# Optimization experiments

Measured on AMD Instinct MI355X. Metric: run time of the kernel, lower is better.

The kernel has to match this reference:

```python
import jax, jax.numpy as jnp
import numpy as np

N_QUBITS = 13
N_LAYERS = 8
DIM = 2 ** N_QUBITS
CDT = jnp.complex64

_X = jnp.array([[0.0, 1.0], [1.0, 0.0]], dtype=CDT)
_Z = jnp.array([[1.0, 0.0], [0.0, -1.0]], dtype=CDT)
_I2 = jnp.eye(2, dtype=CDT)
_CNOT = jnp.array([[1, 0, 0, 0], [0, 1, 0, 0], [0, 0, 0, 1], [0, 0, 1, 0]], dtype=CDT)


def build_ops():
    """Hardware-efficient ansatz: per layer RX on all qubits, RZ on all qubits, CNOT chain."""
    ops = []
    p = 0
    for _ in range(N_LAYERS):
        for q in range(N_QUBITS):
            ops.append(('RX', (q,), p)); p += 1
        for q in range(N_QUBITS):
            ops.append(('RZ', (q,), p)); p += 1
        for q in range(N_QUBITS - 1):
            ops.append(('CNOT', (q, q + 1), None))
    return ops, p

OPS, N_PARAMS = build_ops()


def _rot(generator, theta):
    # U = cos(theta/2) I - i sin(theta/2) G
    h = theta * 0.5
    return jnp.cos(h).astype(CDT) * _I2 - 1j * jnp.sin(h).astype(CDT) * generator


def _apply_1q(state, U, q):
    st = state.reshape((2,) * N_QUBITS)
    st = jnp.tensordot(U, st, axes=([1], [q]))  # contracted axis moves to front
    return jnp.moveaxis(st, 0, q).reshape(-1)


def _apply_2q(state, U, q0, q1):
    st = state.reshape((2,) * N_QUBITS)
    st = jnp.tensordot(U.reshape(2, 2, 2, 2), st, axes=([2, 3], [q0, q1]))
    return jnp.moveaxis(st, (0, 1), (q0, q1)).reshape(-1)


def _run_circuit(params):
    state = jnp.zeros(DIM, dtype=CDT).at[0].set(1.0)
    for gate, qubits, pidx in OPS:
        if gate == 'RX':
            state = _apply_1q(state, _rot(_X, params[pidx]), qubits[0])
        elif gate == 'RZ':
            state = _apply_1q(state, _rot(_Z, params[pidx]), qubits[0])
        else:  # CNOT
            state = _apply_2q(state, _CNOT, qubits[0], qubits[1])
    return state


def setup_inputs() -> dict:
    key = jax.random.key(0)
    k1, k2 = jax.random.split(key)
    params = jax.random.normal(k1, (N_PARAMS,), dtype=jnp.float32)
    observable = jax.random.normal(k2, (DIM, DIM), dtype=jnp.float32)
    return {"params": params, "observable": observable}


def reference(params, observable) -> jnp.ndarray:
    psi = _run_circuit(params)                      # [2^n] complex64
    obs_psi = observable.astype(CDT) @ psi          # dense observable matvec
    loss = jnp.vdot(psi, obs_psi).real.astype(jnp.float32)  # <psi|O|psi>
    return loss
```

## Files before the change

kernel.cpp:

```cpp
#include <hip/hip_runtime.h>

#define DIM 8192
#define NLAYERS 8
#define SIMT 512
#define QFB 2048
#define QFT 256
#define ROWS_PER_BLOCK 4

typedef float floatx4 __attribute__((ext_vector_type(4)));

__device__ __forceinline__ int swz(int i) { return i ^ ((i >> 4) & 15); }

__global__ __launch_bounds__(SIMT) void sim_kernel(const float* __restrict__ params,
                                                   float* __restrict__ outR,
                                                   float* __restrict__ outM) {
    __shared__ float2 buf[2][DIM];
    const int t = threadIdx.x;

    float2 a[16];
#pragma unroll
    for (int l = 0; l < 16; ++l) a[l] = make_float2(0.f, 0.f);
    if (t == 0) a[0].x = 1.f;

    int pp = 0;

    for (int layer = 0; layer < NLAYERS; ++layer) {
        const float* __restrict__ prx = params + layer * 26;
        const float* __restrict__ prz = prx + 13;

        float cb[13], sb[13];
#pragma unroll
        for (int p = 0; p < 13; ++p) __sincosf(0.5f * prx[12 - p], &sb[p], &cb[p]);

#pragma unroll
        for (int k = 0; k < 4; ++k) {
            const float c = cb[k], s = sb[k];
#pragma unroll
            for (int l0 = 0; l0 < 16; ++l0) {
                if (!(l0 & (1 << k))) {
                    const int l1 = l0 | (1 << k);
                    const float2 a0 = a[l0], a1 = a[l1];
                    a[l0] = make_float2(fmaf(c, a0.x, s * a1.y), fmaf(c, a0.y, -s * a1.x));
                    a[l1] = make_float2(fmaf(c, a1.x, s * a0.y), fmaf(c, a1.y, -s * a0.x));
                }
            }
        }

        {
            float2* __restrict__ B = buf[pp]; pp ^= 1;
#pragma unroll
            for (int l = 0; l < 16; ++l) B[swz((t << 4) | l)] = a[l];
            __syncthreads();
#pragma unroll
            for (int l = 0; l < 16; ++l) a[l] = B[swz((t & 15) | (l << 4) | ((t >> 4) << 8))];
        }

#pragma unroll
        for (int k = 0; k < 4; ++k) {
            const float c = cb[4 + k], s = sb[4 + k];
#pragma unroll
            for (int l0 = 0; l0 < 16; ++l0) {
                if (!(l0 & (1 << k))) {
                    const int l1 = l0 | (1 << k);
                    const float2 a0 = a[l0], a1 = a[l1];
                    a[l0] = make_float2(fmaf(c, a0.x, s * a1.y), fmaf(c, a0.y, -s * a1.x));
                    a[l1] = make_float2(fmaf(c, a1.x, s * a0.y), fmaf(c, a1.y, -s * a0.x));
                }
            }
        }

        {
            float2* __restrict__ B = buf[pp]; pp ^= 1;
#pragma unroll
            for (int l = 0; l < 16; ++l) B[swz((t & 15) | (l << 4) | ((t >> 4) << 8))] = a[l];
            __syncthreads();
#pragma unroll
            for (int l = 0; l < 16; ++l)
                a[l] = B[swz(((t >> 1) & 255) | (l << 8) | ((t & 1) << 12))];
        }

#pragma unroll
        for (int k = 0; k < 4; ++k) {
            const float c = cb[8 + k], s = sb[8 + k];
#pragma unroll
            for (int l0 = 0; l0 < 16; ++l0) {
                if (!(l0 & (1 << k))) {
                    const int l1 = l0 | (1 << k);
                    const float2 a0 = a[l0], a1 = a[l1];
                    a[l0] = make_float2(fmaf(c, a0.x, s * a1.y), fmaf(c, a0.y, -s * a1.x));
                    a[l1] = make_float2(fmaf(c, a1.x, s * a0.y), fmaf(c, a1.y, -s * a0.x));
                }
            }
        }

        {
            const float c = cb[12], s = sb[12];
#pragma unroll
            for (int l = 0; l < 16; ++l) {
                const float ox = __shfl_xor(a[l].x, 1);
                const float oy = __shfl_xor(a[l].y, 1);
                a[l] = make_float2(fmaf(c, a[l].x, s * oy), fmaf(c, a[l].y, -s * ox));
            }
        }

        float hz[13];
#pragma unroll
        for (int p = 0; p < 13; ++p) hz[p] = 0.5f * prz[12 - p];
        float phiT = 0.f;
#pragma unroll
        for (int p = 0; p < 8; ++p) phiT += (((t >> 1) >> p) & 1) ? hz[p] : -hz[p];
        phiT += (t & 1) ? hz[12] : -hz[12];
#pragma unroll
        for (int l = 0; l < 16; ++l) {
            float phi = phiT;
            phi += (l & 1) ? hz[8]  : -hz[8];
            phi += (l & 2) ? hz[9]  : -hz[9];
            phi += (l & 4) ? hz[10] : -hz[10];
            phi += (l & 8) ? hz[11] : -hz[11];
            float sp, cp;
            __sincosf(phi, &sp, &cp);
            a[l] = make_float2(a[l].x * cp - a[l].y * sp, a[l].x * sp + a[l].y * cp);
        }

        {
            float2* __restrict__ B = buf[pp]; pp ^= 1;
#pragma unroll
            for (int l = 0; l < 16; ++l)
                B[swz(((t >> 1) & 255) | (l << 8) | ((t & 1) << 12))] = a[l];
            __syncthreads();
#pragma unroll
            for (int l = 0; l < 16; ++l) {
                const int c0 = (t << 4) | l;
                a[l] = B[swz(c0 ^ (c0 >> 1))];
            }
        }
    }

#pragma unroll
    for (int g = 0; g < 4; ++g) {
        const float4 rv = make_float4(a[4*g].x, a[4*g+1].x, a[4*g+2].x, a[4*g+3].x);
        const float4 mv = make_float4(a[4*g].y, a[4*g+1].y, a[4*g+2].y, a[4*g+3].y);
        ((float4*)outR)[(t << 2) + g] = rv;
        ((float4*)outM)[(t << 2) + g] = mv;
    }
}

__global__ __launch_bounds__(QFT) void quad_kernel(const float* __restrict__ O,
                                                   const float* __restrict__ R,
                                                   const float* __restrict__ M,
                                                   float* __restrict__ partials) {
    const int bi = blockIdx.x;
    const int t  = threadIdx.x;
    const float4* __restrict__ R4 = (const float4*)R;
    const float4* __restrict__ M4 = (const float4*)M;

    float acc = 0.f;
#pragma unroll
    for (int rr = 0; rr < ROWS_PER_BLOCK; ++rr) {
        const int i = bi * ROWS_PER_BLOCK + rr;
        const float ri = R[i];
        const float mi = M[i];
        const floatx4* __restrict__ Or = (const floatx4*)(O + (size_t)i * DIM);
#pragma unroll
        for (int it = 0; it < DIM / 4 / QFT; ++it) {
            const int j4 = t + it * QFT;
            const floatx4 o = __builtin_nontemporal_load(&Or[j4]);
            const float4 rj = R4[j4];
            const float4 mj = M4[j4];
            acc = fmaf(o.x, fmaf(ri, rj.x, mi * mj.x), acc);
            acc = fmaf(o.y, fmaf(ri, rj.y, mi * mj.y), acc);
            acc = fmaf(o.z, fmaf(ri, rj.z, mi * mj.z), acc);
            acc = fmaf(o.w, fmaf(ri, rj.w, mi * mj.w), acc);
        }
    }

#pragma unroll
    for (int off = 32; off > 0; off >>= 1) acc += __shfl_down(acc, off);
    __shared__ float wsum[QFT / 64];
    const int lane = t & 63, w = t >> 6;
    if (lane == 0) wsum[w] = acc;
    __syncthreads();
    if (t == 0) {
        float s = 0.f;
#pragma unroll
        for (int k = 0; k < QFT / 64; ++k) s += wsum[k];
        partials[bi] = s;
    }
}

__global__ __launch_bounds__(256) void reduce_kernel(const float* __restrict__ partials,
                                                     float* __restrict__ out) {
    const int t = threadIdx.x;
    float acc = 0.f;
#pragma unroll
    for (int k = 0; k < QFB / 256; ++k) acc += partials[t + k * 256];
#pragma unroll
    for (int off = 32; off > 0; off >>= 1) acc += __shfl_down(acc, off);
    __shared__ float wsum[4];
    const int lane = t & 63, w = t >> 6;
    if (lane == 0) wsum[w] = acc;
    __syncthreads();
    if (t == 0) out[0] = wsum[0] + wsum[1] + wsum[2] + wsum[3];
}

extern "C" void kernel_launch(void* const* d_in, const int* in_sizes, int n_in,
                              void* d_out, int out_size, void* d_ws, size_t ws_size,
                              hipStream_t stream) {
    const float* params = (const float*)d_in[0];
    const float* O      = (const float*)d_in[1];
    float* out = (float*)d_out;

    float* R        = (float*)d_ws;
    float* M        = R + DIM;
    float* partials = M + DIM;

    sim_kernel<<<1, SIMT, 0, stream>>>(params, R, M);
    quad_kernel<<<QFB, QFT, 0, stream>>>(O, R, M, partials);
    reduce_kernel<<<1, 256, 0, stream>>>(partials, out);
}
```

Measured before the change: 83.99 us.

## Fuse simulation and quadratic form into one cooperative kernel with L2 prefetch

Merges the three kernels into a single cooperative launch. Block 0 runs the state-vector simulation while the other blocks stream the tail of the observable matrix (rows from 2048 on) to warm the cache. After a grid sync, every block computes the quadratic form over 32 rows using register-cached psi and separate real and imaginary dot products, and a second grid sync leads to the final reduction. This hides the serial simulation latency behind observable loading and removes launch gaps, but it relies on the prefetched data surviving in cache and on cooperative grid synchronisation.

```diff
diff --git a/kernel.cpp b/kernel.cpp
--- a/kernel.cpp
+++ b/kernel.cpp
@@ -1,206 +1,220 @@
 #include <hip/hip_runtime.h>
+#include <hip/hip_cooperative_groups.h>
 
 #define DIM 8192
 #define NLAYERS 8
-#define SIMT 512
-#define QFB 2048
-#define QFT 256
-#define ROWS_PER_BLOCK 4
-
-typedef float floatx4 __attribute__((ext_vector_type(4)));
+#define NB 256
+#define NT 512
+#define ROWS_PB (DIM / NB)
+#define PRIME_ROW0 2048
+
+namespace cg = cooperative_groups;
 
 __device__ __forceinline__ int swz(int i) { return i ^ ((i >> 4) & 15); }
 
-__global__ __launch_bounds__(SIMT) void sim_kernel(const float* __restrict__ params,
-                                                   float* __restrict__ outR,
-                                                   float* __restrict__ outM) {
-    __shared__ float2 buf[2][DIM];
-    const int t = threadIdx.x;
-
-    float2 a[16];
-#pragma unroll
-    for (int l = 0; l < 16; ++l) a[l] = make_float2(0.f, 0.f);
-    if (t == 0) a[0].x = 1.f;
-
-    int pp = 0;
-
-    for (int layer = 0; layer < NLAYERS; ++layer) {
-        const float* __restrict__ prx = params + layer * 26;
-        const float* __restrict__ prz = prx + 13;
-
-        float cb[13], sb[13];
-#pragma unroll
-        for (int p = 0; p < 13; ++p) __sincosf(0.5f * prx[12 - p], &sb[p], &cb[p]);
-
-#pragma unroll
-        for (int k = 0; k < 4; ++k) {
-            const float c = cb[k], s = sb[k];
-#pragma unroll
-            for (int l0 = 0; l0 < 16; ++l0) {
-                if (!(l0 & (1 << k))) {
-                    const int l1 = l0 | (1 << k);
-                    const float2 a0 = a[l0], a1 = a[l1];
-                    a[l0] = make_float2(fmaf(c, a0.x, s * a1.y), fmaf(c, a0.y, -s * a1.x));
-                    a[l1] = make_float2(fmaf(c, a1.x, s * a0.y), fmaf(c, a1.y, -s * a0.x));
-                }
-            }
-        }
-
-        {
-            float2* __restrict__ B = buf[pp]; pp ^= 1;
-#pragma unroll
-            for (int l = 0; l < 16; ++l) B[swz((t << 4) | l)] = a[l];
-            __syncthreads();
-#pragma unroll
-            for (int l = 0; l < 16; ++l) a[l] = B[swz((t & 15) | (l << 4) | ((t >> 4) << 8))];
-        }
-
-#pragma unroll
-        for (int k = 0; k < 4; ++k) {
-            const float c = cb[4 + k], s = sb[4 + k];
-#pragma unroll
-            for (int l0 = 0; l0 < 16; ++l0) {
-                if (!(l0 & (1 << k))) {
-                    const int l1 = l0 | (1 << k);
-                    const float2 a0 = a[l0], a1 = a[l1];
-                    a[l0] = make_float2(fmaf(c, a0.x, s * a1.y), fmaf(c, a0.y, -s * a1.x));
-                    a[l1] = make_float2(fmaf(c, a1.x, s * a0.y), fmaf(c, a1.y, -s * a0.x));
-                }
-            }
-        }
-
-        {
-            float2* __restrict__ B = buf[pp]; pp ^= 1;
-#pragma unroll
-            for (int l = 0; l < 16; ++l) B[swz((t & 15) | (l << 4) | ((t >> 4) << 8))] = a[l];
+__global__ __launch_bounds__(NT, 2) void fused_kernel(const float* __restrict__ params,
+                                                      const float* __restrict__ O,
+                                                      float* __restrict__ R,
+                                                      float* __restrict__ M,
+                                                      float* __restrict__ partials,
+                                                      float* __restrict__ out) {
+    __shared__ float2 buf[DIM];
+    __shared__ float wsum[8];
+    const int t   = threadIdx.x;
+    const int bid = blockIdx.x;
+    cg::grid_group grid = cg::this_grid();
+
+    if (bid == 0) {
+        float2 a[16];
+#pragma unroll
+        for (int l = 0; l < 16; ++l) a[l] = make_float2(0.f, 0.f);
+        if (t == 0) a[0].x = 1.f;
+
+        for (int layer = 0; layer < NLAYERS; ++layer) {
+            const float* __restrict__ prx = params + layer * 26;
+            const float* __restrict__ prz = prx + 13;
+
+            float cb[13], sb[13];
+#pragma unroll
+            for (int p = 0; p < 13; ++p) __sincosf(0.5f * prx[12 - p], &sb[p], &cb[p]);
+
+#pragma unroll
+            for (int k = 0; k < 4; ++k) {
+                const float c = cb[k], s = sb[k];
+#pragma unroll
+                for (int l0 = 0; l0 < 16; ++l0) {
+                    if (!(l0 & (1 << k))) {
+                        const int l1 = l0 | (1 << k);
+                        const float2 a0 = a[l0], a1 = a[l1];
+                        a[l0] = make_float2(fmaf(c, a0.x, s * a1.y), fmaf(c, a0.y, -s * a1.x));
+                        a[l1] = make_float2(fmaf(c, a1.x, s * a0.y), fmaf(c, a1.y, -s * a0.x));
+                    }
+                }
+            }
+
+            __syncthreads();
+#pragma unroll
+            for (int l = 0; l < 16; ++l) buf[swz((t << 4) | l)] = a[l];
+            __syncthreads();
+#pragma unroll
+            for (int l = 0; l < 16; ++l) a[l] = buf[swz((t & 15) | (l << 4) | ((t >> 4) << 8))];
+
+#pragma unroll
+            for (int k = 0; k < 4; ++k) {
+                const float c = cb[4 + k], s = sb[4 + k];
+#pragma unroll
+                for (int l0 = 0; l0 < 16; ++l0) {
+                    if (!(l0 & (1 << k))) {
+                        const int l1 = l0 | (1 << k);
+                        const float2 a0 = a[l0], a1 = a[l1];
+                        a[l0] = make_float2(fmaf(c, a0.x, s * a1.y), fmaf(c, a0.y, -s * a1.x));
+                        a[l1] = make_float2(fmaf(c, a1.x, s * a0.y), fmaf(c, a1.y, -s * a0.x));
+                    }
+                }
+            }
+
+            __syncthreads();
+#pragma unroll
+            for (int l = 0; l < 16; ++l) buf[swz((t & 15) | (l << 4) | ((t >> 4) << 8))] = a[l];
             __syncthreads();
 #pragma unroll
             for (int l = 0; l < 16; ++l)
-                a[l] = B[swz(((t >> 1) & 255) | (l << 8) | ((t & 1) << 12))];
-        }
-
-#pragma unroll
-        for (int k = 0; k < 4; ++k) {
-            const float c = cb[8 + k], s = sb[8 + k];
-#pragma unroll
-            for (int l0 = 0; l0 < 16; ++l0) {
-                if (!(l0 & (1 << k))) {
-                    const int l1 = l0 | (1 << k);
-                    const float2 a0 = a[l0], a1 = a[l1];
-                    a[l0] = make_float2(fmaf(c, a0.x, s * a1.y), fmaf(c, a0.y, -s * a1.x));
-                    a[l1] = make_float2(fmaf(c, a1.x, s * a0.y), fmaf(c, a1.y, -s * a0.x));
-                }
-            }
-        }
-
-        {
-            const float c = cb[12], s = sb[12];
+                a[l] = buf[swz(((t >> 1) & 255) | (l << 8) | ((t & 1) << 12))];
+
+#pragma unroll
+            for (int k = 0; k < 4; ++k) {
+                const float c = cb[8 + k], s = sb[8 + k];
+#pragma unroll
+                for (int l0 = 0; l0 < 16; ++l0) {
+                    if (!(l0 & (1 << k))) {
+                        const int l1 = l0 | (1 << k);
+                        const float2 a0 = a[l0], a1 = a[l1];
+                        a[l0] = make_float2(fmaf(c, a0.x, s * a1.y), fmaf(c, a0.y, -s * a1.x));
+                        a[l1] = make_float2(fmaf(c, a1.x, s * a0.y), fmaf(c, a1.y, -s * a0.x));
+                    }
+                }
+            }
+
+            {
+                const float c = cb[12], s = sb[12];
+#pragma unroll
+                for (int l = 0; l < 16; ++l) {
+                    const float ox = __shfl_xor(a[l].x, 1);
+                    const float oy = __shfl_xor(a[l].y, 1);
+                    a[l] = make_float2(fmaf(c, a[l].x, s * oy), fmaf(c, a[l].y, -s * ox));
+                }
+            }
+
+            float hz[13];
+#pragma unroll
+            for (int p = 0; p < 13; ++p) hz[p] = 0.5f * prz[12 - p];
+            float phiT = 0.f;
+#pragma unroll
+            for (int p = 0; p < 8; ++p) phiT += (((t >> 1) >> p) & 1) ? hz[p] : -hz[p];
+            phiT += (t & 1) ? hz[12] : -hz[12];
 #pragma unroll
             for (int l = 0; l < 16; ++l) {
-                const float ox = __shfl_xor(a[l].x, 1);
-                const float oy = __shfl_xor(a[l].y, 1);
-                a[l] = make_float2(fmaf(c, a[l].x, s * oy), fmaf(c, a[l].y, -s * ox));
-            }
-        }
-
-        float hz[13];
-#pragma unroll
-        for (int p = 0; p < 13; ++p) hz[p] = 0.5f * prz[12 - p];
-        float phiT = 0.f;
-#pragma unroll
-        for (int p = 0; p < 8; ++p) phiT += (((t >> 1) >> p) & 1) ? hz[p] : -hz[p];
-        phiT += (t & 1) ? hz[12] : -hz[12];
-#pragma unroll
-        for (int l = 0; l < 16; ++l) {
-            float phi = phiT;
-            phi += (l & 1) ? hz[8]  : -hz[8];
-            phi += (l & 2) ? hz[9]  : -hz[9];
-            phi += (l & 4) ? hz[10] : -hz[10];
-            phi += (l & 8) ? hz[11] : -hz[11];
-            float sp, cp;
-            __sincosf(phi, &sp, &cp);
-            a[l] = make_float2(a[l].x * cp - a[l].y * sp, a[l].x * sp + a[l].y * cp);
-        }
-
-        {
-            float2* __restrict__ B = buf[pp]; pp ^= 1;
+                float phi = phiT;
+                phi += (l & 1) ? hz[8]  : -hz[8];
+                phi += (l & 2) ? hz[9]  : -hz[9];
+                phi += (l & 4) ? hz[10] : -hz[10];
+                phi += (l & 8) ? hz[11] : -hz[11];
+                float sp, cp;
+                __sincosf(phi, &sp, &cp);
+                a[l] = make_float2(a[l].x * cp - a[l].y * sp, a[l].x * sp + a[l].y * cp);
+            }
+
+            __syncthreads();
 #pragma unroll
             for (int l = 0; l < 16; ++l)
-                B[swz(((t >> 1) & 255) | (l << 8) | ((t & 1) << 12))] = a[l];
+                buf[swz(((t >> 1) & 255) | (l << 8) | ((t & 1) << 12))] = a[l];
             __syncthreads();
 #pragma unroll
             for (int l = 0; l < 16; ++l) {
                 const int c0 = (t << 4) | l;
-                a[l] = B[swz(c0 ^ (c0 >> 1))];
-            }
-        }
+                a[l] = buf[swz(c0 ^ (c0 >> 1))];
+            }
+        }
+
+#pragma unroll
+        for (int g = 0; g < 4; ++g) {
+            const float4 rv = make_float4(a[4*g].x, a[4*g+1].x, a[4*g+2].x, a[4*g+3].x);
+            const float4 mv = make_float4(a[4*g].y, a[4*g+1].y, a[4*g+2].y, a[4*g+3].y);
+            ((float4*)R)[(t << 2) + g] = rv;
+            ((float4*)M)[(t << 2) + g] = mv;
+        }
+        __threadfence();
+    } else {
+        const float4* __restrict__ O4 = (const float4*)O;
+        const int Q    = (NB - 1) * NT;
+        const int b4   = (PRIME_ROW0 * DIM) / 4;
+        const int e4   = (DIM * DIM) / 4;
+        const int q    = (bid - 1) * NT + t;
+        float dummy = 0.f;
+        for (int k = 0; k < 97; ++k) {
+            const int idx = b4 + q + k * Q;
+            if (idx < e4) {
+                const float4 v = O4[idx];
+                dummy += v.x + v.y + v.z + v.w;
+            }
+        }
+        asm volatile("" :: "v"(dummy));
     }
 
-#pragma unroll
-    for (int g = 0; g < 4; ++g) {
-        const float4 rv = make_float4(a[4*g].x, a[4*g+1].x, a[4*g+2].x, a[4*g+3].x);
-        const float4 mv = make_float4(a[4*g].y, a[4*g+1].y, a[4*g+2].y, a[4*g+3].y);
-        ((float4*)outR)[(t << 2) + g] = rv;
-        ((float4*)outM)[(t << 2) + g] = mv;
+    grid.sync();
+
+    {
+        const float4* __restrict__ R4 = (const float4*)R;
+        const float4* __restrict__ M4 = (const float4*)M;
+        float4 rj[4], mj[4];
+#pragma unroll
+        for (int it = 0; it < 4; ++it) { rj[it] = R4[t + it * NT]; mj[it] = M4[t + it * NT]; }
+
+        float acc = 0.f;
+#pragma unroll 1
+        for (int r = 0; r < ROWS_PB; ++r) {
+            const int i = bid * ROWS_PB + r;
+            const float ri = R[i];
+            const float mi = M[i];
+            const float4* __restrict__ Or = (const float4*)(O + (size_t)i * DIM);
+            float sR = 0.f, sM = 0.f;
+#pragma unroll
+            for (int it = 0; it < 4; ++it) {
+                const float4 o = Or[t + it * NT];
+                sR = fmaf(o.x, rj[it].x, sR); sR = fmaf(o.y, rj[it].y, sR);
+                sR = fmaf(o.z, rj[it].z, sR); sR = fmaf(o.w, rj[it].w, sR);
+                sM = fmaf(o.x, mj[it].x, sM); sM = fmaf(o.y, mj[it].y, sM);
+                sM = fmaf(o.z, mj[it].z, sM); sM = fmaf(o.w, mj[it].w, sM);
+            }
+            acc = fmaf(ri, sR, acc);
+            acc = fmaf(mi, sM, acc);
+        }
+
+#pragma unroll
+        for (int off = 32; off > 0; off >>= 1) acc += __shfl_down(acc, off);
+        __syncthreads();
+        if ((t & 63) == 0) wsum[t >> 6] = acc;
+        __syncthreads();
+        if (t == 0) {
+            float s = 0.f;
+#pragma unroll
+            for (int k = 0; k < 8; ++k) s += wsum[k];
+            partials[bid] = s;
+        }
+        __threadfence();
     }
-}
-
-__global__ __launch_bounds__(QFT) void quad_kernel(const float* __restrict__ O,
-                                                   const float* __restrict__ R,
-                                                   const float* __restrict__ M,
-                                                   float* __restrict__ partials) {
-    const int bi = blockIdx.x;
-    const int t  = threadIdx.x;
-    const float4* __restrict__ R4 = (const float4*)R;
-    const float4* __restrict__ M4 = (const float4*)M;
-
-    float acc = 0.f;
-#pragma unroll
-    for (int rr = 0; rr < ROWS_PER_BLOCK; ++rr) {
-        const int i = bi * ROWS_PER_BLOCK + rr;
-        const float ri = R[i];
-        const float mi = M[i];
-        const floatx4* __restrict__ Or = (const floatx4*)(O + (size_t)i * DIM);
-#pragma unroll
-        for (int it = 0; it < DIM / 4 / QFT; ++it) {
-            const int j4 = t + it * QFT;
-            const floatx4 o = __builtin_nontemporal_load(&Or[j4]);
-            const float4 rj = R4[j4];
-            const float4 mj = M4[j4];
-            acc = fmaf(o.x, fmaf(ri, rj.x, mi * mj.x), acc);
-            acc = fmaf(o.y, fmaf(ri, rj.y, mi * mj.y), acc);
-            acc = fmaf(o.z, fmaf(ri, rj.z, mi * mj.z), acc);
-            acc = fmaf(o.w, fmaf(ri, rj.w, mi * mj.w), acc);
-        }
+
+    grid.sync();
+
+    if (bid == 0) {
+        float v = (t < NB) ? partials[t] : 0.f;
+#pragma unroll
+        for (int off = 32; off > 0; off >>= 1) v += __shfl_down(v, off);
+        __syncthreads();
+        if ((t & 63) == 0) wsum[t >> 6] = v;
+        __syncthreads();
+        if (t == 0) out[0] = wsum[0] + wsum[1] + wsum[2] + wsum[3];
     }
-
-#pragma unroll
-    for (int off = 32; off > 0; off >>= 1) acc += __shfl_down(acc, off);
-    __shared__ float wsum[QFT / 64];
-    const int lane = t & 63, w = t >> 6;
-    if (lane == 0) wsum[w] = acc;
-    __syncthreads();
-    if (t == 0) {
-        float s = 0.f;
-#pragma unroll
-        for (int k = 0; k < QFT / 64; ++k) s += wsum[k];
-        partials[bi] = s;
-    }
-}
-
-__global__ __launch_bounds__(256) void reduce_kernel(const float* __restrict__ partials,
-                                                     float* __restrict__ out) {
-    const int t = threadIdx.x;
-    float acc = 0.f;
-#pragma unroll
-    for (int k = 0; k < QFB / 256; ++k) acc += partials[t + k * 256];
-#pragma unroll
-    for (int off = 32; off > 0; off >>= 1) acc += __shfl_down(acc, off);
-    __shared__ float wsum[4];
-    const int lane = t & 63, w = t >> 6;
-    if (lane == 0) wsum[w] = acc;
-    __syncthreads();
-    if (t == 0) out[0] = wsum[0] + wsum[1] + wsum[2] + wsum[3];
 }
 
 extern "C" void kernel_launch(void* const* d_in, const int* in_sizes, int n_in,
@@ -214,7 +228,8 @@
     float* M        = R + DIM;
     float* partials = M + DIM;
 
-    sim_kernel<<<1, SIMT, 0, stream>>>(params, R, M);
-    quad_kernel<<<QFB, QFT, 0, stream>>>(O, R, M, partials);
-    reduce_kernel<<<1, 256, 0, stream>>>(partials, out);
+    void* args[] = { (void*)&params, (void*)&O, (void*)&R, (void*)&M,
+                     (void*)&partials, (void*)&out };
+    hipLaunchCooperativeKernel((const void*)fused_kernel, dim3(NB), dim3(NT),
+                               args, 0, stream);
 }
```

Measured after the change: 187.7 us. +123.4%, slower.

## Prefetch observable rows into cache with idle blocks during state simulation

Applied to the files above, without the earlier changes.

The simulation kernel now launches 256 blocks instead of 1. Block 0 runs the circuit while the other blocks read the back three-quarters of the observable matrix (rows 2048 onward) and discard the values. The aim is to pull those rows into the last-level cache so the read overlaps the serial simulation. The quad kernel then uses ordinary cached loads for those rows and keeps nontemporal loads for the first 2048 rows. This depends on a 192 MB slice fitting in the MI355X Infinity Cache, which public specs give as 256 MB, and it can contend for bandwidth with the simulation block.

```diff
diff --git a/kernel.cpp b/kernel.cpp
--- a/kernel.cpp
+++ b/kernel.cpp
@@ -3,6 +3,8 @@
 #define DIM 8192
 #define NLAYERS 8
 #define SIMT 512
+#define NB_A 256
+#define PRIME_ROW0 2048
 #define QFB 2048
 #define QFT 256
 #define ROWS_PER_BLOCK 4
@@ -11,11 +13,30 @@
 
 __device__ __forceinline__ int swz(int i) { return i ^ ((i >> 4) & 15); }
 
-__global__ __launch_bounds__(SIMT) void sim_kernel(const float* __restrict__ params,
-                                                   float* __restrict__ outR,
-                                                   float* __restrict__ outM) {
+__global__ __launch_bounds__(SIMT) void simprime_kernel(const float* __restrict__ params,
+                                                        const float* __restrict__ O,
+                                                        float* __restrict__ outR,
+                                                        float* __restrict__ outM) {
     __shared__ float2 buf[2][DIM];
     const int t = threadIdx.x;
+
+    if (blockIdx.x != 0) {
+        const floatx4* __restrict__ O4 = (const floatx4*)O;
+        const int Q  = (NB_A - 1) * SIMT;
+        const int b4 = (PRIME_ROW0 * DIM) / 4;
+        const int e4 = (DIM * DIM) / 4;
+        const int q  = ((int)blockIdx.x - 1) * SIMT + t;
+        float dummy = 0.f;
+        for (int k = 0; k < 97; ++k) {
+            const int idx = b4 + q + k * Q;
+            if (idx < e4) {
+                const floatx4 v = O4[idx];
+                dummy += v.x + v.y + v.z + v.w;
+            }
+        }
+        asm volatile("" :: "v"(dummy));
+        return;
+    }
 
     float2 a[16];
 #pragma unroll
@@ -161,16 +182,30 @@
         const float ri = R[i];
         const float mi = M[i];
         const floatx4* __restrict__ Or = (const floatx4*)(O + (size_t)i * DIM);
-#pragma unroll
-        for (int it = 0; it < DIM / 4 / QFT; ++it) {
-            const int j4 = t + it * QFT;
-            const floatx4 o = __builtin_nontemporal_load(&Or[j4]);
-            const float4 rj = R4[j4];
-            const float4 mj = M4[j4];
-            acc = fmaf(o.x, fmaf(ri, rj.x, mi * mj.x), acc);
-            acc = fmaf(o.y, fmaf(ri, rj.y, mi * mj.y), acc);
-            acc = fmaf(o.z, fmaf(ri, rj.z, mi * mj.z), acc);
-            acc = fmaf(o.w, fmaf(ri, rj.w, mi * mj.w), acc);
+        if (i < PRIME_ROW0) {
+#pragma unroll
+            for (int it = 0; it < DIM / 4 / QFT; ++it) {
+                const int j4 = t + it * QFT;
+                const floatx4 o = __builtin_nontemporal_load(&Or[j4]);
+                const float4 rj = R4[j4];
+                const float4 mj = M4[j4];
+                acc = fmaf(o.x, fmaf(ri, rj.x, mi * mj.x), acc);
+                acc = fmaf(o.y, fmaf(ri, rj.y, mi * mj.y), acc);
+                acc = fmaf(o.z, fmaf(ri, rj.z, mi * mj.z), acc);
+                acc = fmaf(o.w, fmaf(ri, rj.w, mi * mj.w), acc);
+            }
+        } else {
+#pragma unroll
+            for (int it = 0; it < DIM / 4 / QFT; ++it) {
+                const int j4 = t + it * QFT;
+                const floatx4 o = Or[j4];
+                const float4 rj = R4[j4];
+                const float4 mj = M4[j4];
+                acc = fmaf(o.x, fmaf(ri, rj.x, mi * mj.x), acc);
+                acc = fmaf(o.y, fmaf(ri, rj.y, mi * mj.y), acc);
+                acc = fmaf(o.z, fmaf(ri, rj.z, mi * mj.z), acc);
+                acc = fmaf(o.w, fmaf(ri, rj.w, mi * mj.w), acc);
+            }
         }
     }
 
@@ -214,7 +249,7 @@
     float* M        = R + DIM;
     float* partials = M + DIM;
 
-    sim_kernel<<<1, SIMT, 0, stream>>>(params, R, M);
+    simprime_kernel<<<NB_A, SIMT, 0, stream>>>(params, O, R, M);
     quad_kernel<<<QFB, QFT, 0, stream>>>(O, R, M, partials);
     reduce_kernel<<<1, 256, 0, stream>>>(partials, out);
 }
```

Result: no change. 83.40 us (-0.7%).

## Fuse final reduction into quad kernel via last-block atomic counter; vectorize rotations

Applied to the files above, without the earlier changes.

Removes the separate single-block reduce kernel launch. Each quad block publishes its partial, bumps an atomic counter, and the last block to finish sums all partials. The counter is reset inside the simulation kernel. The gate rotations are also rewritten with two-wide float vectors and lane swizzles, so the compiler can emit packed FMA. This adds fence and atomic traffic in exchange for one fewer launch and its kernel boundary.

```diff
diff --git a/kernel.cpp b/kernel.cpp
--- a/kernel.cpp
+++ b/kernel.cpp
@@ -5,22 +5,25 @@
 #define SIMT 512
 #define QFB 2048
 #define QFT 256
-#define ROWS_PER_BLOCK 4
+#define QROWS 4
 
 typedef float floatx4 __attribute__((ext_vector_type(4)));
+typedef float f2 __attribute__((ext_vector_type(2)));
 
 __device__ __forceinline__ int swz(int i) { return i ^ ((i >> 4) & 15); }
 
 __global__ __launch_bounds__(SIMT) void sim_kernel(const float* __restrict__ params,
                                                    float* __restrict__ outR,
-                                                   float* __restrict__ outM) {
-    __shared__ float2 buf[2][DIM];
+                                                   float* __restrict__ outM,
+                                                   unsigned* __restrict__ counter) {
+    __shared__ f2 buf[2][DIM];
     const int t = threadIdx.x;
-
-    float2 a[16];
-#pragma unroll
-    for (int l = 0; l < 16; ++l) a[l] = make_float2(0.f, 0.f);
-    if (t == 0) a[0].x = 1.f;
+    if (t == 0) *counter = 0u;
+
+    f2 a[16];
+#pragma unroll
+    for (int l = 0; l < 16; ++l) a[l] = (f2){0.f, 0.f};
+    if (t == 0) a[0] = (f2){1.f, 0.f};
 
     int pp = 0;
 
@@ -34,20 +37,21 @@
 
 #pragma unroll
         for (int k = 0; k < 4; ++k) {
-            const float c = cb[k], s = sb[k];
+            const f2 c2 = {cb[k], cb[k]};
+            const f2 sg = {sb[k], -sb[k]};
 #pragma unroll
             for (int l0 = 0; l0 < 16; ++l0) {
                 if (!(l0 & (1 << k))) {
                     const int l1 = l0 | (1 << k);
-                    const float2 a0 = a[l0], a1 = a[l1];
-                    a[l0] = make_float2(fmaf(c, a0.x, s * a1.y), fmaf(c, a0.y, -s * a1.x));
-                    a[l1] = make_float2(fmaf(c, a1.x, s * a0.y), fmaf(c, a1.y, -s * a0.x));
+                    const f2 a0 = a[l0], a1 = a[l1];
+                    a[l0] = c2 * a0 + __builtin_shufflevector(a1, a1, 1, 0) * sg;
+                    a[l1] = c2 * a1 + __builtin_shufflevector(a0, a0, 1, 0) * sg;
                 }
             }
         }
 
         {
-            float2* __restrict__ B = buf[pp]; pp ^= 1;
+            f2* __restrict__ B = buf[pp]; pp ^= 1;
 #pragma unroll
             for (int l = 0; l < 16; ++l) B[swz((t << 4) | l)] = a[l];
             __syncthreads();
@@ -57,20 +61,21 @@
 
 #pragma unroll
         for (int k = 0; k < 4; ++k) {
-            const float c = cb[4 + k], s = sb[4 + k];
+            const f2 c2 = {cb[4 + k], cb[4 + k]};
+            const f2 sg = {sb[4 + k], -sb[4 + k]};
 #pragma unroll
             for (int l0 = 0; l0 < 16; ++l0) {
                 if (!(l0 & (1 << k))) {
                     const int l1 = l0 | (1 << k);
-                    const float2 a0 = a[l0], a1 = a[l1];
-                    a[l0] = make_float2(fmaf(c, a0.x, s * a1.y), fmaf(c, a0.y, -s * a1.x));
-                    a[l1] = make_float2(fmaf(c, a1.x, s * a0.y), fmaf(c, a1.y, -s * a0.x));
+                    const f2 a0 = a[l0], a1 = a[l1];
+                    a[l0] = c2 * a0 + __builtin_shufflevector(a1, a1, 1, 0) * sg;
+                    a[l1] = c2 * a1 + __builtin_shufflevector(a0, a0, 1, 0) * sg;
                 }
             }
         }
 
         {
-            float2* __restrict__ B = buf[pp]; pp ^= 1;
+            f2* __restrict__ B = buf[pp]; pp ^= 1;
 #pragma unroll
             for (int l = 0; l < 16; ++l) B[swz((t & 15) | (l << 4) | ((t >> 4) << 8))] = a[l];
             __syncthreads();
@@ -81,25 +86,28 @@
 
 #pragma unroll
         for (int k = 0; k < 4; ++k) {
-            const float c = cb[8 + k], s = sb[8 + k];
+            const f2 c2 = {cb[8 + k], cb[8 + k]};
+            const f2 sg = {sb[8 + k], -sb[8 + k]};
 #pragma unroll
             for (int l0 = 0; l0 < 16; ++l0) {
                 if (!(l0 & (1 << k))) {
                     const int l1 = l0 | (1 << k);
-                    const float2 a0 = a[l0], a1 = a[l1];
-                    a[l0] = make_float2(fmaf(c, a0.x, s * a1.y), fmaf(c, a0.y, -s * a1.x));
-                    a[l1] = make_float2(fmaf(c, a1.x, s * a0.y), fmaf(c, a1.y, -s * a0.x));
+                    const f2 a0 = a[l0], a1 = a[l1];
+                    a[l0] = c2 * a0 + __builtin_shufflevector(a1, a1, 1, 0) * sg;
+                    a[l1] = c2 * a1 + __builtin_shufflevector(a0, a0, 1, 0) * sg;
                 }
             }
         }
 
         {
-            const float c = cb[12], s = sb[12];
+            const f2 c2 = {cb[12], cb[12]};
+            const f2 sg = {sb[12], -sb[12]};
 #pragma unroll
             for (int l = 0; l < 16; ++l) {
-                const float ox = __shfl_xor(a[l].x, 1);
-                const float oy = __shfl_xor(a[l].y, 1);
-                a[l] = make_float2(fmaf(c, a[l].x, s * oy), fmaf(c, a[l].y, -s * ox));
+                f2 o;
+                o.x = __shfl_xor(a[l].x, 1);
+                o.y = __shfl_xor(a[l].y, 1);
+                a[l] = c2 * a[l] + __builtin_shufflevector(o, o, 1, 0) * sg;
             }
         }
 
@@ -119,11 +127,13 @@
             phi += (l & 8) ? hz[11] : -hz[11];
             float sp, cp;
             __sincosf(phi, &sp, &cp);
-            a[l] = make_float2(a[l].x * cp - a[l].y * sp, a[l].x * sp + a[l].y * cp);
-        }
-
-        {
-            float2* __restrict__ B = buf[pp]; pp ^= 1;
+            const f2 c2 = {cp, cp};
+            const f2 sg = {-sp, sp};
+            a[l] = c2 * a[l] + __builtin_shufflevector(a[l], a[l], 1, 0) * sg;
+        }
+
+        {
+            f2* __restrict__ B = buf[pp]; pp ^= 1;
 #pragma unroll
             for (int l = 0; l < 16; ++l)
                 B[swz(((t >> 1) & 255) | (l << 8) | ((t & 1) << 12))] = a[l];
@@ -148,7 +158,9 @@
 __global__ __launch_bounds__(QFT) void quad_kernel(const float* __restrict__ O,
                                                    const float* __restrict__ R,
                                                    const float* __restrict__ M,
-                                                   float* __restrict__ partials) {
+                                                   float* __restrict__ partials,
+                                                   unsigned* __restrict__ counter,
+                                                   float* __restrict__ out) {
     const int bi = blockIdx.x;
     const int t  = threadIdx.x;
     const float4* __restrict__ R4 = (const float4*)R;
@@ -156,8 +168,8 @@
 
     float acc = 0.f;
 #pragma unroll
-    for (int rr = 0; rr < ROWS_PER_BLOCK; ++rr) {
-        const int i = bi * ROWS_PER_BLOCK + rr;
+    for (int rr = 0; rr < QROWS; ++rr) {
+        const int i = bi * QROWS + rr;
         const float ri = R[i];
         const float mi = M[i];
         const floatx4* __restrict__ Or = (const floatx4*)(O + (size_t)i * DIM);
@@ -177,6 +189,7 @@
 #pragma unroll
     for (int off = 32; off > 0; off >>= 1) acc += __shfl_down(acc, off);
     __shared__ float wsum[QFT / 64];
+    __shared__ unsigned lastFlag;
     const int lane = t & 63, w = t >> 6;
     if (lane == 0) wsum[w] = acc;
     __syncthreads();
@@ -185,22 +198,24 @@
 #pragma unroll
         for (int k = 0; k < QFT / 64; ++k) s += wsum[k];
         partials[bi] = s;
-    }
-}
-
-__global__ __launch_bounds__(256) void reduce_kernel(const float* __restrict__ partials,
-                                                     float* __restrict__ out) {
-    const int t = threadIdx.x;
-    float acc = 0.f;
-#pragma unroll
-    for (int k = 0; k < QFB / 256; ++k) acc += partials[t + k * 256];
-#pragma unroll
-    for (int off = 32; off > 0; off >>= 1) acc += __shfl_down(acc, off);
-    __shared__ float wsum[4];
-    const int lane = t & 63, w = t >> 6;
-    if (lane == 0) wsum[w] = acc;
+        __threadfence();
+        lastFlag = (atomicAdd(counter, 1u) == (unsigned)(QFB - 1));
+    }
     __syncthreads();
-    if (t == 0) out[0] = wsum[0] + wsum[1] + wsum[2] + wsum[3];
+
+    if (lastFlag) {
+        float acc2 = 0.f;
+#pragma unroll
+        for (int k = 0; k < QFB / QFT; ++k)
+            acc2 += __hip_atomic_load(&partials[t + k * QFT],
+                                      __ATOMIC_RELAXED, __HIP_MEMORY_SCOPE_AGENT);
+#pragma unroll
+        for (int off = 32; off > 0; off >>= 1) acc2 += __shfl_down(acc2, off);
+        __syncthreads();
+        if (lane == 0) wsum[w] = acc2;
+        __syncthreads();
+        if (t == 0) out[0] = wsum[0] + wsum[1] + wsum[2] + wsum[3];
+    }
 }
 
 extern "C" void kernel_launch(void* const* d_in, const int* in_sizes, int n_in,
@@ -210,11 +225,11 @@
     const float* O      = (const float*)d_in[1];
     float* out = (float*)d_out;
 
-    float* R        = (float*)d_ws;
-    float* M        = R + DIM;
-    float* partials = M + DIM;
-
-    sim_kernel<<<1, SIMT, 0, stream>>>(params, R, M);
-    quad_kernel<<<QFB, QFT, 0, stream>>>(O, R, M, partials);
-    reduce_kernel<<<1, 256, 0, stream>>>(partials, out);
+    float*    R        = (float*)d_ws;
+    float*    M        = R + DIM;
+    float*    partials = M + DIM;
+    unsigned* counter  = (unsigned*)(partials + QFB);
+
+    sim_kernel<<<1, SIMT, 0, stream>>>(params, R, M, counter);
+    quad_kernel<<<QFB, QFT, 0, stream>>>(O, R, M, partials, counter, out);
 }
```

After: 182.5 us. 2.17x slower.
